# Kernel optimization log

Hardware: AMD Instinct MI355X
Metric: run time of the kernel (lower is better)

The kernel has to match this reference:

```python
import jax, jax.numpy as jnp
import numpy as np

B, T, C = 2, 512, 1024   # batch, seq_len, hidden_size
I = 4096                 # expert intermediate size
E = 8                    # num_experts
K = 2                    # top_k


def setup_inputs() -> dict:
    key = jax.random.key(0)
    ks = jax.random.split(key, 8)
    s = 0.02
    return {
        "x": jax.random.normal(ks[0], (B, T, C), jnp.float32),
        # router: Linear(C, C//4) -> ReLU -> Linear(C//4, E)
        "Wr1": jax.random.normal(ks[1], (C, C // 4), jnp.float32) * s,
        "br1": jnp.zeros((C // 4,), jnp.float32),
        "Wr2": jax.random.normal(ks[2], (C // 4, E), jnp.float32) * s,
        "br2": jnp.zeros((E,), jnp.float32),
        # shared expert: Linear(C, I) -> SiLU -> Linear(I, C)
        "Ws1": jax.random.normal(ks[3], (C, I), jnp.float32) * s,
        "bs1": jnp.zeros((I,), jnp.float32),
        "Ws2": jax.random.normal(ks[4], (I, C), jnp.float32) * s,
        "bs2": jnp.zeros((C,), jnp.float32),
        # stacked routed experts
        "We1": jax.random.normal(ks[5], (E, C, I), jnp.float32) * s,
        "be1": jnp.zeros((E, I), jnp.float32),
        "We2": jax.random.normal(ks[6], (E, I, C), jnp.float32) * s,
        "be2": jnp.zeros((E, C), jnp.float32),
    }


def reference(x, Wr1, br1, Wr2, br2, Ws1, bs1, Ws2, bs2, We1, be1, We2, be2):
    Bb, Tt, Cc = x.shape
    xf = x.reshape(-1, Cc)                                  # [N, C]
    # router gates
    logits = jax.nn.relu(xf @ Wr1 + br1) @ Wr2 + br2        # [N, E]
    gates = jax.nn.softmax(logits, axis=-1)
    tg, ti = jax.lax.top_k(gates, K)                        # [N, K]
    tg = jax.nn.softmax(tg / K, axis=-1)                    # re-normalize top-k gates
    # shared expert applied to every token
    out = jax.nn.silu(xf @ Ws1 + bs1) @ Ws2 + bs2           # [N, C]
    # routed experts: loop over the small fixed expert set, mask-combine
    for e in range(E):
        h = jax.nn.silu(xf @ We1[e] + be1[e]) @ We2[e] + be2[e]  # [N, C]
        w = jnp.sum(tg * (ti == e), axis=-1)                     # [N] gate (0 if not routed)
        out = out + w[:, None] * h
    return out.reshape(Bb, Tt, Cc)
```

## Files before the change

kernel.cpp:

```cpp
#include <hip/hip_runtime.h>

#define NTOK 1024
#define CDIM 1024
#define CRDIM 256
#define ENUM 8
#define IDIM 4096
#define WSTRIDE 4194304ull

typedef __bf16 bf16x8 __attribute__((ext_vector_type(8)));
typedef __bf16 bf16x4 __attribute__((ext_vector_type(4)));
typedef float f32x4 __attribute__((ext_vector_type(4)));

typedef const unsigned int __attribute__((address_space(1))) gu32;
typedef unsigned int __attribute__((address_space(3))) lu32;

__device__ __forceinline__ void glds16(const unsigned short* g, unsigned short* l) {
  __builtin_amdgcn_global_load_lds((gu32*)g, (lu32*)l, 16, 0, 0);
}

__device__ __forceinline__ unsigned short f2bf(float f) {
  union { float f; unsigned int u; } v; v.f = f;
  unsigned int r = v.u + 0x7FFFu + ((v.u >> 16) & 1u);
  return (unsigned short)(r >> 16);
}

__global__ __launch_bounds__(256) void init_cast_kernel(
    const float* __restrict__ x, unsigned short* __restrict__ xb) {
  int t = blockIdx.x * 256 + threadIdx.x;
  float4 v = reinterpret_cast<const float4*>(x)[t];
  ushort4 o;
  o.x = f2bf(v.x); o.y = f2bf(v.y); o.z = f2bf(v.z); o.w = f2bf(v.w);
  reinterpret_cast<ushort4*>(xb)[t] = o;
}

#define RT 8
__global__ __launch_bounds__(256) void router_kernel(
    const float* __restrict__ x, const float* __restrict__ Wr1,
    const float* __restrict__ br1, const float* __restrict__ Wr2,
    const float* __restrict__ br2, int* __restrict__ ti,
    float* __restrict__ tw) {
  __shared__ float xs[RT][CDIM];
  __shared__ float hs[RT][CRDIM];
  __shared__ float lg[RT][ENUM];
  const int tid = threadIdx.x;
  const int tok0 = blockIdx.x * RT;
  for (int r = 0; r < RT; ++r) {
    float4 v = reinterpret_cast<const float4*>(x + (size_t)(tok0 + r) * CDIM)[tid];
    *reinterpret_cast<float4*>(&xs[r][tid * 4]) = v;
  }
  __syncthreads();
  float acc[RT];
#pragma unroll
  for (int r = 0; r < RT; ++r) acc[r] = 0.f;
  const int j = tid;
  for (int i = 0; i < CDIM; ++i) {
    float w = Wr1[(size_t)i * CRDIM + j];
#pragma unroll
    for (int r = 0; r < RT; ++r) acc[r] += xs[r][i] * w;
  }
  float b = br1[j];
#pragma unroll
  for (int r = 0; r < RT; ++r) hs[r][j] = fmaxf(acc[r] + b, 0.f);
  __syncthreads();
  if (tid < RT * ENUM) {
    int r = tid >> 3, e = tid & 7;
    float a = 0.f;
    for (int i = 0; i < CRDIM; ++i) a += hs[r][i] * Wr2[(size_t)i * ENUM + e];
    lg[r][e] = a + br2[e];
  }
  __syncthreads();
  if (tid < RT) {
    int r = tid;
    float m = lg[r][0];
#pragma unroll
    for (int e = 1; e < 8; ++e) m = fmaxf(m, lg[r][e]);
    float s = 0.f, g[8];
#pragma unroll
    for (int e = 0; e < 8; ++e) { g[e] = expf(lg[r][e] - m); s += g[e]; }
    float inv = 1.f / s;
    int i0 = 0; float g0 = -1.f;
#pragma unroll
    for (int e = 0; e < 8; ++e) { float ge = g[e] * inv; if (ge > g0) { g0 = ge; i0 = e; } }
    int i1 = 0; float g1 = -2.f;
#pragma unroll
    for (int e = 0; e < 8; ++e) { float ge = g[e] * inv; if (e != i0 && ge > g1) { g1 = ge; i1 = e; } }
    float w0 = 1.f / (1.f + expf((g1 - g0) * 0.5f));
    int n = tok0 + r;
    ti[2 * n] = i0; ti[2 * n + 1] = i1;
    tw[2 * n] = w0; tw[2 * n + 1] = 1.f - w0;
  }
}

__global__ __launch_bounds__(1024) void build_lists_kernel(
    const int* __restrict__ ti, const float* __restrict__ tw,
    int* __restrict__ cnt, int* __restrict__ list, float* __restrict__ gw,
    int* __restrict__ tokslot) {
  __shared__ int s[NTOK];
  const int e = blockIdx.x, n = threadIdx.x;
  int a = ti[2 * n], b = ti[2 * n + 1];
  float w = (a == e) ? tw[2 * n] : ((b == e) ? tw[2 * n + 1] : 0.f);
  int flag = (a == e || b == e) ? 1 : 0;
  s[n] = flag;
  __syncthreads();
  for (int off = 1; off < NTOK; off <<= 1) {
    int v = (n >= off) ? s[n - off] : 0;
    __syncthreads();
    s[n] += v;
    __syncthreads();
  }
  if (flag) {
    int pos = s[n] - 1;
    list[e * NTOK + pos] = n; gw[e * NTOK + pos] = w;
    int slot = (a == e) ? 0 : 1;
    tokslot[2 * n + slot] = (e << 16) | pos;
  }
  if (n == NTOK - 1) cnt[e] = s[n];
}

__global__ void offsets_kernel(const int* __restrict__ cnt, int* __restrict__ offs,
                               int* __restrict__ tbl) {
  if (threadIdx.x == 0) {
    int o = 0;
    for (int e = 0; e < 8; ++e) { offs[e] = o; o += cnt[e]; }
    offs[8] = o;
    int k = 0;
    for (int e = 0; e < 9; ++e) {
      int me = (e < 8) ? cnt[e] : NTOK;
      for (int r0 = 0; r0 < me; r0 += 256) { tbl[1 + k] = e; tbl[41 + k] = r0; ++k; }
    }
    tbl[0] = k;
  }
}

template <int MODE>
__global__ __launch_bounds__(512, 4) void gemm_w(
    const unsigned short* __restrict__ Abase,
    const float* __restrict__ Wr, const float* __restrict__ Wsh,
    const float* __restrict__ br, const float* __restrict__ bsh,
    const int* __restrict__ cnt, const int* __restrict__ offs,
    const int* __restrict__ list,
    unsigned short* __restrict__ Hout, float* __restrict__ pout,
    const int* __restrict__ tbl) {
  __shared__ __align__(16) unsigned short smA[3 * 8192];
  __shared__ __align__(16) unsigned short smB[2 * 5120];
  const int y = blockIdx.y;
  if (y >= tbl[0]) return;
  const int e = tbl[1 + y], row0 = tbl[41 + y];
  const int nt = (MODE == 0) ? blockIdx.x : (blockIdx.x & 7);
  const int kc = (MODE == 0) ? 0 : (blockIdx.x >> 3);

  constexpr int KD = (MODE == 0) ? CDIM : IDIM;
  constexpr int ND = (MODE == 0) ? IDIM : CDIM;
  constexpr int NT = 32;
  const int me = (e < 8) ? cnt[e] : NTOK;
  const int valid = min(256, me - row0);
  const int n0 = nt * 128;
  const float* Bsrc = (e < 8) ? (Wr + (size_t)e * WSTRIDE) : Wsh;
  const float* bias = (e < 8) ? (br + (size_t)e * ND) : bsh;
  const int hbase = (e < 8) ? offs[e] : 2048;
  const int tid = threadIdx.x;
  const int lane = tid & 63, w = tid >> 6;
  const int kbeg = kc * 1024;

  const int rl = lane >> 2, cs = lane & 3;
  const int r0w = 32 * w + rl;
  const int q0 = cs ^ ((r0w >> 1) & 3);
  const int q1 = cs ^ (((r0w + 16) >> 1) & 3);
  int src_r0, src_r1;
  if (MODE == 0) {
    if (e < 8) {
      src_r0 = list[e * NTOK + row0 + min(r0w, valid - 1)];
      src_r1 = list[e * NTOK + row0 + min(r0w + 16, valid - 1)];
    } else {
      src_r0 = row0 + min(r0w, valid - 1);
      src_r1 = row0 + min(r0w + 16, valid - 1);
    }
  } else {
    src_r0 = hbase + row0 + min(r0w, valid - 1);
    src_r1 = hbase + row0 + min(r0w + 16, valid - 1);
  }
  const unsigned short* srcA0 = Abase + (size_t)src_r0 * KD + kbeg + q0 * 8;
  const unsigned short* srcA1 = Abase + (size_t)src_r1 * KD + kbeg + q1 * 8;
  const int aB0 = (32 * w) * 32;
  const int aB1 = (32 * w + 16) * 32;

  const int c4 = (tid & 31) * 4;
  const int kp = tid >> 5;
  const float* srcB = Bsrc + (size_t)(kbeg + 2 * kp) * ND + n0 + c4;

  const int wr = (w >> 1) * 64, wc = (w & 1) * 64;
  const int lr = lane & 15, q = lane >> 4;
  int offA[4], offB0[4];
#pragma unroll
  for (int m = 0; m < 4; ++m) {
    int R = wr + m * 16 + lr;
    offA[m] = R * 32 + (q ^ ((R >> 1) & 3)) * 8;
  }
#pragma unroll
  for (int n = 0; n < 4; ++n) {
    int R = wc + n * 16 + lr;
    int u = (R >> 3) & 7;
    offB0[n] = R * 40 + ((2 * q) ^ u) * 4;
  }

  f32x4 acc[4][4];
#pragma unroll
  for (int m = 0; m < 4; ++m)
#pragma unroll
    for (int n = 0; n < 4; ++n) acc[m][n] = (f32x4)0.f;

  unsigned short *ca = smA, *na = smA + 8192, *wa = smA + 16384;
  unsigned short *bc = smB, *bn = smB + 5120;
  f32x4 rbA[2], rbB[2];

#define ASTG(T, BA)                                       \
  {                                                       \
    glds16(srcA0 + (size_t)(T) * 32, (BA) + aB0);         \
    glds16(srcA1 + (size_t)(T) * 32, (BA) + aB1);         \
  }
#define BLOAD(T, R)                                       \
  {                                                       \
    const float* bp = srcB + (size_t)(T) * 32 * ND;       \
    R[0] = *reinterpret_cast<const f32x4*>(bp);           \
    R[1] = *reinterpret_cast<const f32x4*>(bp + ND);      \
  }
#define BWRITE(R, BB)                                                          \
  {                                                                            \
    _Pragma("unroll") for (int j = 0; j < 4; ++j) {                            \
      int col = c4 + j;                                                        \
      int kp2 = kp ^ (2 * ((col >> 3) & 7));                                   \
      unsigned int pk =                                                        \
          (unsigned int)__builtin_bit_cast(unsigned short, (__bf16)R[0][j]) |  \
          ((unsigned int)__builtin_bit_cast(unsigned short, (__bf16)R[1][j])   \
           << 16);                                                             \
      *reinterpret_cast<unsigned int*>((BB) + col * 40 + kp2 * 2) = pk;        \
    }                                                                          \
  }
#define MFMAS()                                                                \
  {                                                                            \
    bf16x8 av[4];                                                              \
    _Pragma("unroll") for (int m = 0; m < 4; ++m)                              \
        av[m] = *reinterpret_cast<const bf16x8*>(ca + offA[m]);                \
    _Pragma("unroll") for (int n = 0; n < 4; ++n) {                            \
      bf16x4 lo = *reinterpret_cast<const bf16x4*>(bc + offB0[n]);             \
      bf16x4 hi = *reinterpret_cast<const bf16x4*>(bc + (offB0[n] ^ 4));       \
      bf16x8 bv = __builtin_shufflevector(lo, hi, 0, 1, 2, 3, 4, 5, 6, 7);     \
      _Pragma("unroll") for (int m = 0; m < 4; ++m)                            \
          acc[m][n] = __builtin_amdgcn_mfma_f32_16x16x32_bf16(av[m], bv,       \
                                                              acc[m][n], 0,   \
                                                              0, 0);           \
    }                                                                          \
  }

  ASTG(0, ca); BLOAD(0, rbA);
  __builtin_amdgcn_sched_barrier(0);
  ASTG(1, na); BLOAD(1, rbB);
  asm volatile("s_waitcnt vmcnt(4)" ::: "memory");
  __builtin_amdgcn_sched_barrier(0);
  BWRITE(rbA, bc);
  asm volatile("s_waitcnt lgkmcnt(0)" ::: "memory");
  __builtin_amdgcn_s_barrier();
  __builtin_amdgcn_sched_barrier(0);

#define GBODY(T, RL, RW)                                                     \
  {                                                                          \
    if ((T) + 2 < NT) { ASTG((T) + 2, wa); BLOAD((T) + 2, RL); }             \
    MFMAS();                                                                 \
    if ((T) + 1 < NT) {                                                      \
      if ((T) + 2 < NT) {                                                    \
        asm volatile("s_waitcnt vmcnt(4)" ::: "memory");                     \
      } else {                                                               \
        asm volatile("s_waitcnt vmcnt(0)" ::: "memory");                     \
      }                                                                      \
      __builtin_amdgcn_sched_barrier(0);                                     \
      BWRITE(RW, bn);                                                        \
      asm volatile("s_waitcnt lgkmcnt(0)" ::: "memory");                     \
      __builtin_amdgcn_s_barrier();                                          \
      __builtin_amdgcn_sched_barrier(0);                                     \
    }                                                                        \
    { unsigned short* tp = ca; ca = na; na = wa; wa = tp; }                  \
    { unsigned short* tp = bc; bc = bn; bn = tp; }                           \
  }

  for (int t = 0; t < NT; t += 2) {
    GBODY(t, rbA, rbB)
    GBODY(t + 1, rbB, rbA)
  }
#undef GBODY
#undef MFMAS
#undef BWRITE
#undef BLOAD
#undef ASTG

  const int rbase = wr + (q << 2);
#pragma unroll
  for (int n = 0; n < 4; ++n) {
    const int col = n0 + wc + n * 16 + lr;
    const float bval = (MODE == 0 || kc == 0) ? bias[col] : 0.f;
#pragma unroll
    for (int m = 0; m < 4; ++m) {
#pragma unroll
      for (int r = 0; r < 4; ++r) {
        const int i = rbase + m * 16 + r;
        if (i < valid) {
          float v = acc[m][n][r] + bval;
          if (MODE == 0) {
            float sv = v / (1.f + __expf(-v));
            Hout[(size_t)(hbase + row0 + i) * IDIM + col] = f2bf(sv);
          } else {
            pout[((size_t)kc * 3072 + hbase + row0 + i) * CDIM + col] = v;
          }
        }
      }
    }
  }
}

__global__ __launch_bounds__(256) void reduce_kernel(
    const float* __restrict__ pout, const int* __restrict__ tokslot,
    const float* __restrict__ tw, const int* __restrict__ offs,
    float* __restrict__ out) {
  const int tok = blockIdx.x;
  const int c = threadIdx.x * 4;
  const int t0 = tokslot[2 * tok], t1 = tokslot[2 * tok + 1];
  const float g0 = tw[2 * tok], g1 = tw[2 * tok + 1];
  const int r0 = offs[t0 >> 16] + (t0 & 0xffff);
  const int r1 = offs[t1 >> 16] + (t1 & 0xffff);
  const int rs = 2048 + tok;
  float4 acc; acc.x = 0.f; acc.y = 0.f; acc.z = 0.f; acc.w = 0.f;
#pragma unroll
  for (int kc = 0; kc < 4; ++kc) {
    const float* base = pout + (size_t)kc * 3072 * CDIM;
    float4 a = *reinterpret_cast<const float4*>(base + (size_t)rs * CDIM + c);
    float4 b = *reinterpret_cast<const float4*>(base + (size_t)r0 * CDIM + c);
    float4 d = *reinterpret_cast<const float4*>(base + (size_t)r1 * CDIM + c);
    acc.x += a.x + g0 * b.x + g1 * d.x;
    acc.y += a.y + g0 * b.y + g1 * d.y;
    acc.z += a.z + g0 * b.z + g1 * d.z;
    acc.w += a.w + g0 * b.w + g1 * d.w;
  }
  *reinterpret_cast<float4*>(out + (size_t)tok * CDIM + c) = acc;
}

extern "C" void kernel_launch(void* const* d_in, const int* in_sizes, int n_in,
                              void* d_out, int out_size, void* d_ws, size_t ws_size,
                              hipStream_t stream) {
  const float* x = (const float*)d_in[0];
  const float* Wr1 = (const float*)d_in[1];
  const float* br1 = (const float*)d_in[2];
  const float* Wr2 = (const float*)d_in[3];
  const float* br2 = (const float*)d_in[4];
  const float* Ws1 = (const float*)d_in[5];
  const float* bs1 = (const float*)d_in[6];
  const float* Ws2 = (const float*)d_in[7];
  const float* bs2 = (const float*)d_in[8];
  const float* We1 = (const float*)d_in[9];
  const float* be1 = (const float*)d_in[10];
  const float* We2 = (const float*)d_in[11];
  const float* be2 = (const float*)d_in[12];
  float* out = (float*)d_out;

  char* ws = (char*)d_ws;
  unsigned short* xb = (unsigned short*)(ws + 0);
  int* ti = (int*)(ws + 2097152);
  float* tw = (float*)(ws + 2105344);
  int* cnt = (int*)(ws + 2113536);
  int* offs = (int*)(ws + 2113792);
  int* list = (int*)(ws + 2114048);
  float* gw = (float*)(ws + 2146816);
  unsigned short* H = (unsigned short*)(ws + 2179584);
  int* tbl = (int*)(ws + 27345408);
  int* tokslot = (int*)(ws + 27345920);
  float* pout = (float*)(ws + 27354112ull);

  init_cast_kernel<<<1024, 256, 0, stream>>>(x, xb);
  router_kernel<<<NTOK / RT, 256, 0, stream>>>(x, Wr1, br1, Wr2, br2, ti, tw);
  build_lists_kernel<<<8, 1024, 0, stream>>>(ti, tw, cnt, list, gw, tokslot);
  offsets_kernel<<<1, 64, 0, stream>>>(cnt, offs, tbl);
  gemm_w<0><<<dim3(32, 20), 512, 0, stream>>>(xb, We1, Ws1, be1, bs1, cnt, offs,
                                              list, H, nullptr, tbl);
  gemm_w<1><<<dim3(32, 20), 512, 0, stream>>>(H, We2, Ws2, be2, bs2, cnt, offs,
                                              nullptr, nullptr, pout, tbl);
  reduce_kernel<<<1024, 256, 0, stream>>>(pout, tokslot, tw, offs, out);
}
```

Baseline: 239.9 us.

## Halve GEMM M-tile to 128 rows, simplify pipeline, fuse cast with router

The GEMM tiles shrink from 256 to 128 token rows, with a 2x4 warp layout of 64x32 per warp. The grid's y dimension doubles to 40 and launch bounds allow more resident blocks. The three-stage A pipeline with two B register sets becomes a simple double buffer that waits on vmcnt(0) every step. The fp32->bf16 cast and the router now share one prep kernel, and the router reads x straight from global memory instead of shared memory. The aim is less padding waste on uneven per-expert token counts, more blocks in flight, and one fewer launch, at the cost of more B-weight rereads per token and less latency hiding in the loop.

Result: slower. 377.3 us (+57.3%).

```diff
diff --git a/kernel.cpp b/kernel.cpp
--- a/kernel.cpp
+++ b/kernel.cpp
@@ -24,39 +24,25 @@
   return (unsigned short)(r >> 16);
 }
 
-__global__ __launch_bounds__(256) void init_cast_kernel(
-    const float* __restrict__ x, unsigned short* __restrict__ xb) {
-  int t = blockIdx.x * 256 + threadIdx.x;
-  float4 v = reinterpret_cast<const float4*>(x)[t];
-  ushort4 o;
-  o.x = f2bf(v.x); o.y = f2bf(v.y); o.z = f2bf(v.z); o.w = f2bf(v.w);
-  reinterpret_cast<ushort4*>(xb)[t] = o;
-}
-
 #define RT 8
-__global__ __launch_bounds__(256) void router_kernel(
-    const float* __restrict__ x, const float* __restrict__ Wr1,
+__device__ __forceinline__ void router_block(
+    int rb, const float* __restrict__ x, const float* __restrict__ Wr1,
     const float* __restrict__ br1, const float* __restrict__ Wr2,
-    const float* __restrict__ br2, int* __restrict__ ti,
-    float* __restrict__ tw) {
-  __shared__ float xs[RT][CDIM];
-  __shared__ float hs[RT][CRDIM];
-  __shared__ float lg[RT][ENUM];
+    const float* __restrict__ br2, int* __restrict__ ti, float* __restrict__ tw,
+    char* pool) {
+  float (*hs)[CRDIM] = (float(*)[CRDIM])pool;
+  float (*lg)[ENUM] = (float(*)[ENUM])(pool + 8192);
   const int tid = threadIdx.x;
-  const int tok0 = blockIdx.x * RT;
-  for (int r = 0; r < RT; ++r) {
-    float4 v = reinterpret_cast<const float4*>(x + (size_t)(tok0 + r) * CDIM)[tid];
-    *reinterpret_cast<float4*>(&xs[r][tid * 4]) = v;
-  }
-  __syncthreads();
+  const int tok0 = rb * RT;
   float acc[RT];
 #pragma unroll
   for (int r = 0; r < RT; ++r) acc[r] = 0.f;
   const int j = tid;
+  const float* xrow = x + (size_t)tok0 * CDIM;
   for (int i = 0; i < CDIM; ++i) {
     float w = Wr1[(size_t)i * CRDIM + j];
 #pragma unroll
-    for (int r = 0; r < RT; ++r) acc[r] += xs[r][i] * w;
+    for (int r = 0; r < RT; ++r) acc[r] += xrow[r * CDIM + i] * w;
   }
   float b = br1[j];
 #pragma unroll
@@ -88,6 +74,24 @@
     int n = tok0 + r;
     ti[2 * n] = i0; ti[2 * n + 1] = i1;
     tw[2 * n] = w0; tw[2 * n + 1] = 1.f - w0;
+  }
+}
+
+__global__ __launch_bounds__(256) void prep_kernel(
+    const float* __restrict__ x, unsigned short* __restrict__ xb,
+    const float* __restrict__ Wr1, const float* __restrict__ br1,
+    const float* __restrict__ Wr2, const float* __restrict__ br2,
+    int* __restrict__ ti, float* __restrict__ tw) {
+  __shared__ __align__(16) char pool[8448];
+  const int b = blockIdx.x;
+  if (b < 1024) {
+    int t = b * 256 + threadIdx.x;
+    float4 v = reinterpret_cast<const float4*>(x)[t];
+    ushort4 o;
+    o.x = f2bf(v.x); o.y = f2bf(v.y); o.z = f2bf(v.z); o.w = f2bf(v.w);
+    reinterpret_cast<ushort4*>(xb)[t] = o;
+  } else {
+    router_block(b - 1024, x, Wr1, br1, Wr2, br2, ti, tw, pool);
   }
 }
 
@@ -126,14 +130,14 @@
     int k = 0;
     for (int e = 0; e < 9; ++e) {
       int me = (e < 8) ? cnt[e] : NTOK;
-      for (int r0 = 0; r0 < me; r0 += 256) { tbl[1 + k] = e; tbl[41 + k] = r0; ++k; }
+      for (int r0 = 0; r0 < me; r0 += 128) { tbl[1 + k] = e; tbl[41 + k] = r0; ++k; }
     }
     tbl[0] = k;
   }
 }
 
 template <int MODE>
-__global__ __launch_bounds__(512, 4) void gemm_w(
+__global__ __launch_bounds__(512, 8) void gemm_w(
     const unsigned short* __restrict__ Abase,
     const float* __restrict__ Wr, const float* __restrict__ Wsh,
     const float* __restrict__ br, const float* __restrict__ bsh,
@@ -141,7 +145,7 @@
     const int* __restrict__ list,
     unsigned short* __restrict__ Hout, float* __restrict__ pout,
     const int* __restrict__ tbl) {
-  __shared__ __align__(16) unsigned short smA[3 * 8192];
+  __shared__ __align__(16) unsigned short smA[2 * 4096];
   __shared__ __align__(16) unsigned short smB[2 * 5120];
   const int y = blockIdx.y;
   if (y >= tbl[0]) return;
@@ -153,7 +157,7 @@
   constexpr int ND = (MODE == 0) ? IDIM : CDIM;
   constexpr int NT = 32;
   const int me = (e < 8) ? cnt[e] : NTOK;
-  const int valid = min(256, me - row0);
+  const int valid = min(128, me - row0);
   const int n0 = nt * 128;
   const float* Bsrc = (e < 8) ? (Wr + (size_t)e * WSTRIDE) : Wsh;
   const float* bias = (e < 8) ? (br + (size_t)e * ND) : bsh;
@@ -163,75 +167,62 @@
   const int kbeg = kc * 1024;
 
   const int rl = lane >> 2, cs = lane & 3;
-  const int r0w = 32 * w + rl;
-  const int q0 = cs ^ ((r0w >> 1) & 3);
-  const int q1 = cs ^ (((r0w + 16) >> 1) & 3);
-  int src_r0, src_r1;
+  const int rw = 16 * w + rl;
+  const int qa = cs ^ ((rw >> 1) & 3);
+  int src_r;
   if (MODE == 0) {
-    if (e < 8) {
-      src_r0 = list[e * NTOK + row0 + min(r0w, valid - 1)];
-      src_r1 = list[e * NTOK + row0 + min(r0w + 16, valid - 1)];
-    } else {
-      src_r0 = row0 + min(r0w, valid - 1);
-      src_r1 = row0 + min(r0w + 16, valid - 1);
-    }
+    src_r = (e < 8) ? list[e * NTOK + row0 + min(rw, valid - 1)]
+                    : (row0 + min(rw, valid - 1));
   } else {
-    src_r0 = hbase + row0 + min(r0w, valid - 1);
-    src_r1 = hbase + row0 + min(r0w + 16, valid - 1);
-  }
-  const unsigned short* srcA0 = Abase + (size_t)src_r0 * KD + kbeg + q0 * 8;
-  const unsigned short* srcA1 = Abase + (size_t)src_r1 * KD + kbeg + q1 * 8;
-  const int aB0 = (32 * w) * 32;
-  const int aB1 = (32 * w + 16) * 32;
+    src_r = hbase + row0 + min(rw, valid - 1);
+  }
+  const unsigned short* srcA = Abase + (size_t)src_r * KD + kbeg + qa * 8;
+  const int aB = (16 * w) * 32;
 
   const int c4 = (tid & 31) * 4;
   const int kp = tid >> 5;
   const float* srcB = Bsrc + (size_t)(kbeg + 2 * kp) * ND + n0 + c4;
 
-  const int wr = (w >> 1) * 64, wc = (w & 1) * 64;
+  const int wr = (w >> 2) * 64, wc = (w & 3) * 32;
   const int lr = lane & 15, q = lane >> 4;
-  int offA[4], offB0[4];
+  int offA[4], offB0[2];
 #pragma unroll
   for (int m = 0; m < 4; ++m) {
     int R = wr + m * 16 + lr;
     offA[m] = R * 32 + (q ^ ((R >> 1) & 3)) * 8;
   }
 #pragma unroll
-  for (int n = 0; n < 4; ++n) {
+  for (int n = 0; n < 2; ++n) {
     int R = wc + n * 16 + lr;
     int u = (R >> 3) & 7;
     offB0[n] = R * 40 + ((2 * q) ^ u) * 4;
   }
 
-  f32x4 acc[4][4];
+  f32x4 acc[4][2];
 #pragma unroll
   for (int m = 0; m < 4; ++m)
 #pragma unroll
-    for (int n = 0; n < 4; ++n) acc[m][n] = (f32x4)0.f;
-
-  unsigned short *ca = smA, *na = smA + 8192, *wa = smA + 16384;
+    for (int n = 0; n < 2; ++n) acc[m][n] = (f32x4)0.f;
+
+  unsigned short *ca = smA, *na = smA + 4096;
   unsigned short *bc = smB, *bn = smB + 5120;
-  f32x4 rbA[2], rbB[2];
-
-#define ASTG(T, BA)                                       \
-  {                                                       \
-    glds16(srcA0 + (size_t)(T) * 32, (BA) + aB0);         \
-    glds16(srcA1 + (size_t)(T) * 32, (BA) + aB1);         \
-  }
-#define BLOAD(T, R)                                       \
-  {                                                       \
-    const float* bp = srcB + (size_t)(T) * 32 * ND;       \
-    R[0] = *reinterpret_cast<const f32x4*>(bp);           \
-    R[1] = *reinterpret_cast<const f32x4*>(bp + ND);      \
-  }
-#define BWRITE(R, BB)                                                          \
+  f32x4 rb[2];
+
+#define ASTG(T, BA) { glds16(srcA + (size_t)(T) * 32, (BA) + aB); }
+#define BLOAD(T)                                        \
+  {                                                     \
+    const float* bp = srcB + (size_t)(T) * 32 * ND;     \
+    rb[0] = *reinterpret_cast<const f32x4*>(bp);        \
+    rb[1] = *reinterpret_cast<const f32x4*>(bp + ND);   \
+  }
+#define BWRITE(BB)                                                             \
   {                                                                            \
     _Pragma("unroll") for (int j = 0; j < 4; ++j) {                            \
       int col = c4 + j;                                                        \
       int kp2 = kp ^ (2 * ((col >> 3) & 7));                                   \
       unsigned int pk =                                                        \
-          (unsigned int)__builtin_bit_cast(unsigned short, (__bf16)R[0][j]) |  \
-          ((unsigned int)__builtin_bit_cast(unsigned short, (__bf16)R[1][j])   \
+          (unsigned int)__builtin_bit_cast(unsigned short, (__bf16)rb[0][j]) | \
+          ((unsigned int)__builtin_bit_cast(unsigned short, (__bf16)rb[1][j])  \
            << 16);                                                             \
       *reinterpret_cast<unsigned int*>((BB) + col * 40 + kp2 * 2) = pk;        \
     }                                                                          \
@@ -241,7 +232,7 @@
     bf16x8 av[4];                                                              \
     _Pragma("unroll") for (int m = 0; m < 4; ++m)                              \
         av[m] = *reinterpret_cast<const bf16x8*>(ca + offA[m]);                \
-    _Pragma("unroll") for (int n = 0; n < 4; ++n) {                            \
+    _Pragma("unroll") for (int n = 0; n < 2; ++n) {                            \
       bf16x4 lo = *reinterpret_cast<const bf16x4*>(bc + offB0[n]);             \
       bf16x4 hi = *reinterpret_cast<const bf16x4*>(bc + (offB0[n] ^ 4));       \
       bf16x8 bv = __builtin_shufflevector(lo, hi, 0, 1, 2, 3, 4, 5, 6, 7);     \
@@ -252,41 +243,30 @@
     }                                                                          \
   }
 
-  ASTG(0, ca); BLOAD(0, rbA);
+  ASTG(0, ca); BLOAD(0);
+  asm volatile("s_waitcnt vmcnt(0)" ::: "memory");
   __builtin_amdgcn_sched_barrier(0);
-  ASTG(1, na); BLOAD(1, rbB);
-  asm volatile("s_waitcnt vmcnt(4)" ::: "memory");
-  __builtin_amdgcn_sched_barrier(0);
-  BWRITE(rbA, bc);
+  BWRITE(bc);
   asm volatile("s_waitcnt lgkmcnt(0)" ::: "memory");
   __builtin_amdgcn_s_barrier();
   __builtin_amdgcn_sched_barrier(0);
 
-#define GBODY(T, RL, RW)                                                     \
-  {                                                                          \
-    if ((T) + 2 < NT) { ASTG((T) + 2, wa); BLOAD((T) + 2, RL); }             \
-    MFMAS();                                                                 \
-    if ((T) + 1 < NT) {                                                      \
-      if ((T) + 2 < NT) {                                                    \
-        asm volatile("s_waitcnt vmcnt(4)" ::: "memory");                     \
-      } else {                                                               \
-        asm volatile("s_waitcnt vmcnt(0)" ::: "memory");                     \
-      }                                                                      \
-      __builtin_amdgcn_sched_barrier(0);                                     \
-      BWRITE(RW, bn);                                                        \
-      asm volatile("s_waitcnt lgkmcnt(0)" ::: "memory");                     \
-      __builtin_amdgcn_s_barrier();                                          \
-      __builtin_amdgcn_sched_barrier(0);                                     \
-    }                                                                        \
-    { unsigned short* tp = ca; ca = na; na = wa; wa = tp; }                  \
-    { unsigned short* tp = bc; bc = bn; bn = tp; }                           \
-  }
-
-  for (int t = 0; t < NT; t += 2) {
-    GBODY(t, rbA, rbB)
-    GBODY(t + 1, rbB, rbA)
-  }
-#undef GBODY
+  for (int t = 0; t < NT; ++t) {
+    if (t + 1 < NT) { ASTG(t + 1, na); BLOAD(t + 1); }
+    __builtin_amdgcn_sched_barrier(0);
+    MFMAS();
+    __builtin_amdgcn_sched_barrier(0);
+    if (t + 1 < NT) {
+      asm volatile("s_waitcnt vmcnt(0)" ::: "memory");
+      __builtin_amdgcn_sched_barrier(0);
+      BWRITE(bn);
+    }
+    asm volatile("s_waitcnt lgkmcnt(0)" ::: "memory");
+    __builtin_amdgcn_s_barrier();
+    __builtin_amdgcn_sched_barrier(0);
+    { unsigned short* tp = ca; ca = na; na = tp; }
+    { unsigned short* tp = bc; bc = bn; bn = tp; }
+  }
 #undef MFMAS
 #undef BWRITE
 #undef BLOAD
@@ -294,7 +274,7 @@
 
   const int rbase = wr + (q << 2);
 #pragma unroll
-  for (int n = 0; n < 4; ++n) {
+  for (int n = 0; n < 2; ++n) {
     const int col = n0 + wc + n * 16 + lr;
     const float bval = (MODE == 0 || kc == 0) ? bias[col] : 0.f;
 #pragma unroll
@@ -373,13 +353,12 @@
   int* tokslot = (int*)(ws + 27345920);
   float* pout = (float*)(ws + 27354112ull);
 
-  init_cast_kernel<<<1024, 256, 0, stream>>>(x, xb);
-  router_kernel<<<NTOK / RT, 256, 0, stream>>>(x, Wr1, br1, Wr2, br2, ti, tw);
+  prep_kernel<<<1152, 256, 0, stream>>>(x, xb, Wr1, br1, Wr2, br2, ti, tw);
   build_lists_kernel<<<8, 1024, 0, stream>>>(ti, tw, cnt, list, gw, tokslot);
   offsets_kernel<<<1, 64, 0, stream>>>(cnt, offs, tbl);
-  gemm_w<0><<<dim3(32, 20), 512, 0, stream>>>(xb, We1, Ws1, be1, bs1, cnt, offs,
+  gemm_w<0><<<dim3(32, 40), 512, 0, stream>>>(xb, We1, Ws1, be1, bs1, cnt, offs,
                                               list, H, nullptr, tbl);
-  gemm_w<1><<<dim3(32, 20), 512, 0, stream>>>(H, We2, Ws2, be2, bs2, cnt, offs,
+  gemm_w<1><<<dim3(32, 40), 512, 0, stream>>>(H, We2, Ws2, be2, bs2, cnt, offs,
                                               nullptr, nullptr, pout, tbl);
   reduce_kernel<<<1024, 256, 0, stream>>>(pout, tokslot, tw, offs, out);
 }
```

## Merge cast and router into one prep kernel, drop offsets kernel

Applied to the files above, without the earlier changes.

Combines the fp32-to-bf16 cast and the router into a single launch, where extra blocks run the router on 16 tokens each and read x directly from global memory instead of staging it in shared memory. Removes the single-thread offsets kernel: each GEMM block now derives its expert, row start and H base from the counts, and reduce computes prefix offsets inline. The unused gate-weight list is dropped. This cuts the launch count from seven to five, at the cost of redundant prefix sums per block and uncached global reads of x in the router.

Result: slower. 377.9 us (+57.5%).

```diff
diff --git a/kernel.cpp b/kernel.cpp
--- a/kernel.cpp
+++ b/kernel.cpp
@@ -24,39 +24,25 @@
   return (unsigned short)(r >> 16);
 }
 
-__global__ __launch_bounds__(256) void init_cast_kernel(
-    const float* __restrict__ x, unsigned short* __restrict__ xb) {
-  int t = blockIdx.x * 256 + threadIdx.x;
-  float4 v = reinterpret_cast<const float4*>(x)[t];
-  ushort4 o;
-  o.x = f2bf(v.x); o.y = f2bf(v.y); o.z = f2bf(v.z); o.w = f2bf(v.w);
-  reinterpret_cast<ushort4*>(xb)[t] = o;
-}
-
-#define RT 8
-__global__ __launch_bounds__(256) void router_kernel(
-    const float* __restrict__ x, const float* __restrict__ Wr1,
+#define RT 16
+__device__ __forceinline__ void router_block(
+    int rb, const float* __restrict__ x, const float* __restrict__ Wr1,
     const float* __restrict__ br1, const float* __restrict__ Wr2,
-    const float* __restrict__ br2, int* __restrict__ ti,
-    float* __restrict__ tw) {
-  __shared__ float xs[RT][CDIM];
-  __shared__ float hs[RT][CRDIM];
-  __shared__ float lg[RT][ENUM];
+    const float* __restrict__ br2, int* __restrict__ ti, float* __restrict__ tw,
+    char* pool) {
+  float (*hs)[CRDIM] = (float(*)[CRDIM])pool;
+  float (*lg)[ENUM] = (float(*)[ENUM])(pool + 16384);
   const int tid = threadIdx.x;
-  const int tok0 = blockIdx.x * RT;
-  for (int r = 0; r < RT; ++r) {
-    float4 v = reinterpret_cast<const float4*>(x + (size_t)(tok0 + r) * CDIM)[tid];
-    *reinterpret_cast<float4*>(&xs[r][tid * 4]) = v;
-  }
-  __syncthreads();
+  const int tok0 = rb * RT;
   float acc[RT];
 #pragma unroll
   for (int r = 0; r < RT; ++r) acc[r] = 0.f;
   const int j = tid;
+  const float* xrow = x + (size_t)tok0 * CDIM;
   for (int i = 0; i < CDIM; ++i) {
     float w = Wr1[(size_t)i * CRDIM + j];
 #pragma unroll
-    for (int r = 0; r < RT; ++r) acc[r] += xs[r][i] * w;
+    for (int r = 0; r < RT; ++r) acc[r] += xrow[r * CDIM + i] * w;
   }
   float b = br1[j];
 #pragma unroll
@@ -91,14 +77,30 @@
   }
 }
 
+__global__ __launch_bounds__(256) void prep_kernel(
+    const float* __restrict__ x, unsigned short* __restrict__ xb,
+    const float* __restrict__ Wr1, const float* __restrict__ br1,
+    const float* __restrict__ Wr2, const float* __restrict__ br2,
+    int* __restrict__ ti, float* __restrict__ tw) {
+  __shared__ __align__(16) char pool[16896];
+  const int b = blockIdx.x;
+  if (b < 1024) {
+    int t = b * 256 + threadIdx.x;
+    float4 v = reinterpret_cast<const float4*>(x)[t];
+    ushort4 o;
+    o.x = f2bf(v.x); o.y = f2bf(v.y); o.z = f2bf(v.z); o.w = f2bf(v.w);
+    reinterpret_cast<ushort4*>(xb)[t] = o;
+  } else {
+    router_block(b - 1024, x, Wr1, br1, Wr2, br2, ti, tw, pool);
+  }
+}
+
 __global__ __launch_bounds__(1024) void build_lists_kernel(
     const int* __restrict__ ti, const float* __restrict__ tw,
-    int* __restrict__ cnt, int* __restrict__ list, float* __restrict__ gw,
-    int* __restrict__ tokslot) {
+    int* __restrict__ cnt, int* __restrict__ list, int* __restrict__ tokslot) {
   __shared__ int s[NTOK];
   const int e = blockIdx.x, n = threadIdx.x;
   int a = ti[2 * n], b = ti[2 * n + 1];
-  float w = (a == e) ? tw[2 * n] : ((b == e) ? tw[2 * n + 1] : 0.f);
   int flag = (a == e || b == e) ? 1 : 0;
   s[n] = flag;
   __syncthreads();
@@ -110,26 +112,33 @@
   }
   if (flag) {
     int pos = s[n] - 1;
-    list[e * NTOK + pos] = n; gw[e * NTOK + pos] = w;
+    list[e * NTOK + pos] = n;
     int slot = (a == e) ? 0 : 1;
     tokslot[2 * n + slot] = (e << 16) | pos;
   }
   if (n == NTOK - 1) cnt[e] = s[n];
 }
 
-__global__ void offsets_kernel(const int* __restrict__ cnt, int* __restrict__ offs,
-                               int* __restrict__ tbl) {
-  if (threadIdx.x == 0) {
-    int o = 0;
-    for (int e = 0; e < 8; ++e) { offs[e] = o; o += cnt[e]; }
-    offs[8] = o;
-    int k = 0;
-    for (int e = 0; e < 9; ++e) {
-      int me = (e < 8) ? cnt[e] : NTOK;
-      for (int r0 = 0; r0 < me; r0 += 256) { tbl[1 + k] = e; tbl[41 + k] = r0; ++k; }
+__device__ __forceinline__ bool tile_lookup(const int* __restrict__ cnt, int y,
+                                            int& e_out, int& row0_out,
+                                            int& hbase_out) {
+  int c[8];
+#pragma unroll
+  for (int i = 0; i < 8; ++i) c[i] = cnt[i];
+  int k = 0, found = -1, r0 = 0, pre = 0, hb = 0;
+#pragma unroll
+  for (int ee = 0; ee < 9; ++ee) {
+    int me = (ee < 8) ? c[ee] : NTOK;
+    int nt_e = (me + 255) >> 8;
+    if (found < 0 && y < k + nt_e) {
+      found = ee; r0 = (y - k) << 8; hb = (ee < 8) ? pre : 2048;
     }
-    tbl[0] = k;
-  }
+    k += nt_e;
+    if (ee < 8) pre += me;
+  }
+  if (found < 0) return false;
+  e_out = found; row0_out = r0; hbase_out = hb;
+  return true;
 }
 
 template <int MODE>
@@ -137,15 +146,12 @@
     const unsigned short* __restrict__ Abase,
     const float* __restrict__ Wr, const float* __restrict__ Wsh,
     const float* __restrict__ br, const float* __restrict__ bsh,
-    const int* __restrict__ cnt, const int* __restrict__ offs,
-    const int* __restrict__ list,
-    unsigned short* __restrict__ Hout, float* __restrict__ pout,
-    const int* __restrict__ tbl) {
+    const int* __restrict__ cnt, const int* __restrict__ list,
+    unsigned short* __restrict__ Hout, float* __restrict__ pout) {
   __shared__ __align__(16) unsigned short smA[3 * 8192];
   __shared__ __align__(16) unsigned short smB[2 * 5120];
-  const int y = blockIdx.y;
-  if (y >= tbl[0]) return;
-  const int e = tbl[1 + y], row0 = tbl[41 + y];
+  int e, row0, hbase;
+  if (!tile_lookup(cnt, blockIdx.y, e, row0, hbase)) return;
   const int nt = (MODE == 0) ? blockIdx.x : (blockIdx.x & 7);
   const int kc = (MODE == 0) ? 0 : (blockIdx.x >> 3);
 
@@ -157,7 +163,6 @@
   const int n0 = nt * 128;
   const float* Bsrc = (e < 8) ? (Wr + (size_t)e * WSTRIDE) : Wsh;
   const float* bias = (e < 8) ? (br + (size_t)e * ND) : bsh;
-  const int hbase = (e < 8) ? offs[e] : 2048;
   const int tid = threadIdx.x;
   const int lane = tid & 63, w = tid >> 6;
   const int kbeg = kc * 1024;
@@ -318,10 +323,16 @@
 
 __global__ __launch_bounds__(256) void reduce_kernel(
     const float* __restrict__ pout, const int* __restrict__ tokslot,
-    const float* __restrict__ tw, const int* __restrict__ offs,
+    const float* __restrict__ tw, const int* __restrict__ cnt,
     float* __restrict__ out) {
   const int tok = blockIdx.x;
   const int c = threadIdx.x * 4;
+  int offs[8];
+  {
+    int o = 0;
+#pragma unroll
+    for (int e = 0; e < 8; ++e) { offs[e] = o; o += cnt[e]; }
+  }
   const int t0 = tokslot[2 * tok], t1 = tokslot[2 * tok + 1];
   const float g0 = tw[2 * tok], g1 = tw[2 * tok + 1];
   const int r0 = offs[t0 >> 16] + (t0 & 0xffff);
@@ -365,21 +376,16 @@
   int* ti = (int*)(ws + 2097152);
   float* tw = (float*)(ws + 2105344);
   int* cnt = (int*)(ws + 2113536);
-  int* offs = (int*)(ws + 2113792);
   int* list = (int*)(ws + 2114048);
-  float* gw = (float*)(ws + 2146816);
   unsigned short* H = (unsigned short*)(ws + 2179584);
-  int* tbl = (int*)(ws + 27345408);
   int* tokslot = (int*)(ws + 27345920);
   float* pout = (float*)(ws + 27354112ull);
 
-  init_cast_kernel<<<1024, 256, 0, stream>>>(x, xb);
-  router_kernel<<<NTOK / RT, 256, 0, stream>>>(x, Wr1, br1, Wr2, br2, ti, tw);
-  build_lists_kernel<<<8, 1024, 0, stream>>>(ti, tw, cnt, list, gw, tokslot);
-  offsets_kernel<<<1, 64, 0, stream>>>(cnt, offs, tbl);
-  gemm_w<0><<<dim3(32, 20), 512, 0, stream>>>(xb, We1, Ws1, be1, bs1, cnt, offs,
-                                              list, H, nullptr, tbl);
-  gemm_w<1><<<dim3(32, 20), 512, 0, stream>>>(H, We2, Ws2, be2, bs2, cnt, offs,
-                                              nullptr, nullptr, pout, tbl);
-  reduce_kernel<<<1024, 256, 0, stream>>>(pout, tokslot, tw, offs, out);
-}
+  prep_kernel<<<1088, 256, 0, stream>>>(x, xb, Wr1, br1, Wr2, br2, ti, tw);
+  build_lists_kernel<<<8, 1024, 0, stream>>>(ti, tw, cnt, list, tokslot);
+  gemm_w<0><<<dim3(32, 20), 512, 0, stream>>>(xb, We1, Ws1, be1, bs1, cnt, list,
+                                              H, nullptr);
+  gemm_w<1><<<dim3(32, 20), 512, 0, stream>>>(H, We2, Ws2, be2, bs2, cnt, list,
+                                              nullptr, pout);
+  reduce_kernel<<<1024, 256, 0, stream>>>(pout, tokslot, tw, cnt, out);
+}
```
